# Optimization experiments

Measured on AMD Instinct MI355X. Metric: run time of the kernel, lower is better.

## Reference

```python
import jax, jax.numpy as jnp
import numpy as np

N = 50000; E = 800000; IN = 256; HID = 128; H = 4; C = 32; L = 3
REL = 100; RD = 16; EH = 32  # rel_emb_dim, edge-encoder hidden
LN_EPS = 1e-5


def _ln(x, g, b):
    m = jnp.mean(x, axis=-1, keepdims=True)
    v = jnp.mean((x - m) ** 2, axis=-1, keepdims=True)
    return (x - m) * jax.lax.rsqrt(v + LN_EPS) * g + b


def _mlp2(x, W1, b1, W2, b2):
    return jax.nn.relu(x @ W1 + b1) @ W2 + b2


def _forward(x, edge_attr, in_g, in_b, proj_W, proj_b,
             dist_W1, dist_b1, dist_W2, dist_b2,
             coexp_W1, coexp_b1, coexp_W2, coexp_b2,
             rel_emb, fus_W1, fus_b1, fus_ln_g, fus_ln_b, fus_W2, fus_b2,
             Wsrc, Wdst, Wedge, att, sscale, ng, nb, edge_index):
    src, dst = edge_index[0], edge_index[1]
    dist_w = edge_attr[:, 0]                              # [E] raw distance weight
    # ---- edge encoder ----
    dist_feat = _mlp2(edge_attr[:, 0:1], dist_W1, dist_b1, dist_W2, dist_b2)   # [E,RD]
    coexp_feat = _mlp2(edge_attr[:, 1:2], coexp_W1, coexp_b1, coexp_W2, coexp_b2)
    rel_id = jnp.clip(edge_attr[:, 2].astype(jnp.int32), 0, REL - 1)
    rel_feat = rel_emb[rel_id]                            # [E,RD]
    comb = jnp.concatenate([dist_feat, coexp_feat, rel_feat], axis=1)          # [E,3*RD]
    h = comb @ fus_W1 + fus_b1
    h = jax.nn.relu(_ln(h, fus_ln_g, fus_ln_b))
    edge_feat = h @ fus_W2 + fus_b2                       # [E,RD]
    # ---- input norm + projection ----
    x = _ln(x, in_g, in_b) @ proj_W + proj_b              # [N,HID]
    # ---- GAT layers ----
    for i in range(L):
        x_res = x
        xs = (x @ Wsrc[i]).reshape(N, H, C)
        xd = (x @ Wdst[i]).reshape(N, H, C)
        ef = (edge_feat @ Wedge[i]).reshape(E, H, C)
        a = jnp.tanh(xs[src] + xd[dst] + ef)              # [E,H,C]
        alpha = jnp.sum(a * att[i][None], axis=-1)        # [E,H]
        if i < L - 1:  # spatial_decay on all but last layer
            alpha = alpha * (dist_w[:, None] ** sscale[i][None, :])
        amax = jax.ops.segment_max(alpha, dst, num_segments=N)   # [N,H]
        ea = jnp.exp(alpha - amax[dst])
        esum = jax.ops.segment_sum(ea, dst, num_segments=N)
        alpha = ea / (esum[dst] + 1e-8)                   # [E,H]
        msg = xs[src] * alpha[..., None]                  # [E,H,C]
        out = jax.ops.segment_sum(msg, dst, num_segments=N).reshape(N, H * C)
        x = jax.nn.elu(_ln(out, ng[i], nb[i])) + x_res
    return x


def setup_inputs() -> dict:
    key = jax.random.key(0)
    ks = jax.random.split(key, 24)
    p = lambda k, s: jax.random.normal(k, s, jnp.float32) * 0.05
    edge_attr = jnp.concatenate([
        jax.random.uniform(ks[2], (E, 2), jnp.float32, 0.01, 1.0),
        jax.random.randint(ks[3], (E, 1), 0, REL).astype(jnp.float32)], axis=1)
    return dict(
        x=jax.random.normal(ks[0], (N, IN), jnp.float32),
        edge_index=jax.random.randint(ks[1], (2, E), 0, N),
        edge_attr=edge_attr,
        in_g=jnp.ones((IN,), jnp.float32), in_b=jnp.zeros((IN,), jnp.float32),
        proj_W=p(ks[4], (IN, HID)), proj_b=jnp.zeros((HID,), jnp.float32),
        dist_W1=p(ks[5], (1, EH)), dist_b1=jnp.zeros((EH,), jnp.float32),
        dist_W2=p(ks[6], (EH, RD)), dist_b2=jnp.zeros((RD,), jnp.float32),
        coexp_W1=p(ks[7], (1, EH)), coexp_b1=jnp.zeros((EH,), jnp.float32),
        coexp_W2=p(ks[8], (EH, RD)), coexp_b2=jnp.zeros((RD,), jnp.float32),
        rel_emb=p(ks[9], (REL, RD)),
        fus_W1=p(ks[10], (3 * RD, 2 * RD)), fus_b1=jnp.zeros((2 * RD,), jnp.float32),
        fus_ln_g=jnp.ones((2 * RD,), jnp.float32), fus_ln_b=jnp.zeros((2 * RD,), jnp.float32),
        fus_W2=p(ks[11], (2 * RD, RD)), fus_b2=jnp.zeros((RD,), jnp.float32),
        Wsrc=p(ks[12], (L, HID, HID)), Wdst=p(ks[13], (L, HID, HID)),
        Wedge=p(ks[14], (L, RD, HID)), att=p(ks[15], (L, H, C)),
        sscale=jnp.ones((L, H), jnp.float32),
        ng=jnp.ones((L, HID), jnp.float32), nb=jnp.zeros((L, HID), jnp.float32),
    )


def reference(x, edge_index, edge_attr, in_g, in_b, proj_W, proj_b,
              dist_W1, dist_b1, dist_W2, dist_b2,
              coexp_W1, coexp_b1, coexp_W2, coexp_b2,
              rel_emb, fus_W1, fus_b1, fus_ln_g, fus_ln_b, fus_W2, fus_b2,
              Wsrc, Wdst, Wedge, att, sscale, ng, nb):
    return _forward(x, edge_attr, in_g, in_b, proj_W, proj_b,
                    dist_W1, dist_b1, dist_W2, dist_b2,
                    coexp_W1, coexp_b1, coexp_W2, coexp_b2,
                    rel_emb, fus_W1, fus_b1, fus_ln_g, fus_ln_b, fus_W2, fus_b2,
                    Wsrc, Wdst, Wedge, att, sscale, ng, nb, edge_index)
```

## Files before the change

kernel.cpp:

```cpp
#include <hip/hip_runtime.h>
#include <math.h>

#define NN 50000
#define NE 800000
#define IND 256
#define HD 128
#define NH 4
#define NC 32
#define RELN 100
#define RD 16
#define EHD 32

typedef unsigned int uint;
typedef _Float16 half2_t __attribute__((ext_vector_type(2)));

__device__ inline uint pack_bf16(float a, float b) {
    uint ua = __float_as_uint(a), ub = __float_as_uint(b);
    ua += 0x7fffu + ((ua >> 16) & 1u);
    ub += 0x7fffu + ((ub >> 16) & 1u);
    return (ua >> 16) | (ub & 0xffff0000u);
}

__device__ inline uint pack_f16(float a, float b) {
    half2_t h = { (_Float16)a, (_Float16)b };
    return __builtin_bit_cast(uint, h);
}

#if __has_builtin(__builtin_amdgcn_fdot2)
#define FDOT2(a, b, c) __builtin_amdgcn_fdot2((a), (b), (c), false)
#else
static __device__ inline float FDOT2(half2_t a, half2_t b, float c) {
    return c + (float)a.x * (float)b.x + (float)a.y * (float)b.y;
}
#endif

__device__ inline float dpp_add(float a, const int ctrl) {
    int t;
    switch (ctrl) {
        case 0: t = __builtin_amdgcn_update_dpp(0, __float_as_int(a), 0xB1,  0xF, 0xF, true); break;
        case 1: t = __builtin_amdgcn_update_dpp(0, __float_as_int(a), 0x4E,  0xF, 0xF, true); break;
        case 2: t = __builtin_amdgcn_update_dpp(0, __float_as_int(a), 0x141, 0xF, 0xF, true); break;
        default:t = __builtin_amdgcn_update_dpp(0, __float_as_int(a), 0x140, 0xF, 0xF, true); break;
    }
    return a + __int_as_float(t);
}
__device__ inline float dpp_reduce16(float a) {
    a = dpp_add(a, 0);
    a = dpp_add(a, 1);
    a = dpp_add(a, 2);
    a = dpp_add(a, 3);
    return a;
}

__global__ __launch_bounds__(256) void count_kernel(
    const int* __restrict__ dst, int* __restrict__ counts)
{
    int e = blockIdx.x * 256 + threadIdx.x;
    if (e < NE) atomicAdd(&counts[dst[e]], 1);
}

__global__ __launch_bounds__(1024) void scan_a_kernel(
    const int* __restrict__ counts, int* __restrict__ row_ptr,
    int* __restrict__ partials, int n)
{
    __shared__ int wsum[16];
    int tid = threadIdx.x;
    int i = blockIdx.x * 1024 + tid;
    int v = (i < n) ? counts[i] : 0;
    int lane = tid & 63;
    int incl = v;
#pragma unroll
    for (int off = 1; off < 64; off <<= 1) {
        int t = __shfl_up(incl, off);
        if (lane >= off) incl += t;
    }
    if (lane == 63) wsum[tid >> 6] = incl;
    __syncthreads();
    if (tid < 16) {
        int w = wsum[tid];
        int inc2 = w;
#pragma unroll
        for (int off = 1; off < 16; off <<= 1) {
            int u = __shfl_up(inc2, off);
            if (tid >= off) inc2 += u;
        }
        wsum[tid] = inc2 - w;
    }
    __syncthreads();
    int excl = wsum[tid >> 6] + incl - v;
    if (i < n) row_ptr[i] = excl;
    if (tid == 1023) partials[blockIdx.x] = excl + v;
}

__global__ __launch_bounds__(64) void scan_b_kernel(
    int* __restrict__ partials, int* __restrict__ row_ptr, int nblk, int n)
{
    int tid = threadIdx.x;
    int v = (tid < nblk) ? partials[tid] : 0;
    int incl = v;
#pragma unroll
    for (int off = 1; off < 64; off <<= 1) {
        int t = __shfl_up(incl, off);
        if (tid >= off) incl += t;
    }
    if (tid < nblk) partials[tid] = incl - v;
    if (tid == nblk - 1) row_ptr[n] = incl;
}

__global__ __launch_bounds__(1024) void scan_c_kernel(
    int* __restrict__ row_ptr, int* __restrict__ cursor,
    const int* __restrict__ partials, int n)
{
    int i = blockIdx.x * 1024 + threadIdx.x;
    if (i < n) {
        int r = row_ptr[i] + partials[blockIdx.x];
        row_ptr[i] = r;
        cursor[i] = r;
    }
}

__global__ __launch_bounds__(256) void edge_feat_fill_kernel(
    const float* __restrict__ eattr, const int* __restrict__ src,
    const int* __restrict__ dst, int* __restrict__ cursor,
    const float* __restrict__ dW1, const float* __restrict__ db1,
    const float* __restrict__ dW2, const float* __restrict__ db2,
    const float* __restrict__ cW1, const float* __restrict__ cb1,
    const float* __restrict__ cW2, const float* __restrict__ cb2,
    const float* __restrict__ rel_emb,
    const float* __restrict__ fW1, const float* __restrict__ fb1,
    const float* __restrict__ fg,  const float* __restrict__ fbl,
    const float* __restrict__ fW2, const float* __restrict__ fb2,
    uint4* __restrict__ efeat_h, int2* __restrict__ meta_c)
{
    int e = blockIdx.x * 256 + threadIdx.x;
    if (e >= NE) return;
    float d  = eattr[(size_t)e * 3 + 0];
    float cx = eattr[(size_t)e * 3 + 1];
    int r = (int)eattr[(size_t)e * 3 + 2];
    r = min(max(r, 0), RELN - 1);
    int p = atomicAdd(&cursor[dst[e]], 1);
    meta_c[p] = make_int2(src[e], __float_as_int(__log2f(d)));

    float df[RD], cf[RD];
#pragma unroll
    for (int k = 0; k < RD; k++) { df[k] = db2[k]; cf[k] = cb2[k]; }
    for (int j = 0; j < EHD; j++) {
        float h1 = fmaxf(d  * dW1[j] + db1[j], 0.f);
        float h2 = fmaxf(cx * cW1[j] + cb1[j], 0.f);
#pragma unroll
        for (int k = 0; k < RD; k++) {
            df[k] += h1 * dW2[j * RD + k];
            cf[k] += h2 * cW2[j * RD + k];
        }
    }
    float hh[2 * RD];
#pragma unroll
    for (int m = 0; m < 2 * RD; m++) hh[m] = fb1[m];
    for (int k = 0; k < RD; k++) {
        float a = df[k], b = cf[k], c = rel_emb[r * RD + k];
#pragma unroll
        for (int m = 0; m < 2 * RD; m++) {
            hh[m] += a * fW1[k * (2 * RD) + m]
                   + b * fW1[(RD + k) * (2 * RD) + m]
                   + c * fW1[(2 * RD + k) * (2 * RD) + m];
        }
    }
    float s = 0.f;
#pragma unroll
    for (int m = 0; m < 2 * RD; m++) s += hh[m];
    float mean = s * (1.f / (2 * RD));
    float s2 = 0.f;
#pragma unroll
    for (int m = 0; m < 2 * RD; m++) { float dd = hh[m] - mean; s2 += dd * dd; }
    float rs = rsqrtf(s2 * (1.f / (2 * RD)) + 1e-5f);
#pragma unroll
    for (int m = 0; m < 2 * RD; m++)
        hh[m] = fmaxf((hh[m] - mean) * rs * fg[m] + fbl[m], 0.f);

    float ef[RD];
#pragma unroll
    for (int k = 0; k < RD; k++) ef[k] = fb2[k];
    for (int m = 0; m < 2 * RD; m++) {
        float hv = hh[m];
#pragma unroll
        for (int k = 0; k < RD; k++) ef[k] += hv * fW2[m * RD + k];
    }
    uint4 e0, e1;
    e0.x = pack_f16(ef[0],  ef[1]);  e0.y = pack_f16(ef[2],  ef[3]);
    e0.z = pack_f16(ef[4],  ef[5]);  e0.w = pack_f16(ef[6],  ef[7]);
    e1.x = pack_f16(ef[8],  ef[9]);  e1.y = pack_f16(ef[10], ef[11]);
    e1.z = pack_f16(ef[12], ef[13]); e1.w = pack_f16(ef[14], ef[15]);
    efeat_h[(size_t)p * 2 + 0] = e0;
    efeat_h[(size_t)p * 2 + 1] = e1;
}

__global__ __launch_bounds__(256) void ln_proj_kernel(
    const float* __restrict__ x, const float* __restrict__ g, const float* __restrict__ b,
    const float* __restrict__ W, const float* __restrict__ pb, float* __restrict__ x0)
{
    __shared__ float xr[8][IND];
    __shared__ float mv[8][2];
    int nb = blockIdx.x * 8;
    int tid = threadIdx.x;
    const float4* xv = (const float4*)(x + (size_t)nb * IND);
    float4* xl = (float4*)&xr[0][0];
    xl[tid] = xv[tid];
    xl[tid + 256] = xv[tid + 256];
    __syncthreads();
    int node = tid >> 5, lane = tid & 31;
    float s1 = 0.f, s2 = 0.f;
#pragma unroll
    for (int j = 0; j < 8; j++) { float v = xr[node][lane + 32 * j]; s1 += v; s2 += v * v; }
#pragma unroll
    for (int off = 16; off >= 1; off >>= 1) { s1 += __shfl_xor(s1, off); s2 += __shfl_xor(s2, off); }
    if (lane == 0) {
        float mean = s1 * (1.f / IND);
        mv[node][0] = mean;
        mv[node][1] = rsqrtf(s2 * (1.f / IND) - mean * mean + 1e-5f);
    }
    __syncthreads();
#pragma unroll
    for (int j = 0; j < 8; j++) {
        int k = lane + 32 * j;
        xr[node][k] = (xr[node][k] - mv[node][0]) * mv[node][1] * g[k] + b[k];
    }
    __syncthreads();
    int col = tid & 127, r0 = (tid >> 7) * 4;
    float acc[4] = {0.f, 0.f, 0.f, 0.f};
    for (int k = 0; k < IND; k += 4) {
        float4 x4[4];
#pragma unroll
        for (int r = 0; r < 4; r++) x4[r] = *(const float4*)&xr[r0 + r][k];
        float w0 = W[(k + 0) * HD + col];
        float w1 = W[(k + 1) * HD + col];
        float w2 = W[(k + 2) * HD + col];
        float w3 = W[(k + 3) * HD + col];
#pragma unroll
        for (int r = 0; r < 4; r++)
            acc[r] += x4[r].x * w0 + x4[r].y * w1 + x4[r].z * w2 + x4[r].w * w3;
    }
    float pbv = pb[col];
#pragma unroll
    for (int r = 0; r < 4; r++)
        x0[(size_t)(nb + r0 + r) * HD + col] = acc[r] + pbv;
}

__global__ __launch_bounds__(512) void gemm_sd_kernel(
    const float* __restrict__ x, const float* __restrict__ Ws, const float* __restrict__ Wd,
    uint* __restrict__ xs_p, float2* __restrict__ xd2)
{
    __shared__ float xt[32][HD];
    int nb = blockIdx.x * 32;
    int tid = threadIdx.x;
    const float4* xv = (const float4*)(x + (size_t)nb * HD);
    float4* xl = (float4*)&xt[0][0];
    int validf4 = (NN - nb >= 32) ? 1024 : (NN - nb) * 32;
#pragma unroll
    for (int u = 0; u < 2; u++) {
        int idx = tid + u * 512;
        float4 v = {0.f, 0.f, 0.f, 0.f};
        if (idx < validf4) v = xv[idx];
        xl[idx] = v;
    }
    __syncthreads();
    int half = tid >> 8;
    int t = tid & 255;
    int q = t & 31;
    int r0 = (t >> 5) * 4;
    const float4* W4 = (const float4*)(half ? Wd : Ws);
    float4 acc[4] = { {0,0,0,0}, {0,0,0,0}, {0,0,0,0}, {0,0,0,0} };
    for (int k = 0; k < HD; k += 4) {
        float4 xr[4];
#pragma unroll
        for (int r = 0; r < 4; r++) xr[r] = *(const float4*)&xt[r0 + r][k];
        float4 w0 = W4[(k + 0) * 32 + q];
        float4 w1 = W4[(k + 1) * 32 + q];
        float4 w2 = W4[(k + 2) * 32 + q];
        float4 w3 = W4[(k + 3) * 32 + q];
#pragma unroll
        for (int r = 0; r < 4; r++) {
            acc[r].x += xr[r].x * w0.x + xr[r].y * w1.x + xr[r].z * w2.x + xr[r].w * w3.x;
            acc[r].y += xr[r].x * w0.y + xr[r].y * w1.y + xr[r].z * w2.y + xr[r].w * w3.y;
            acc[r].z += xr[r].x * w0.z + xr[r].y * w1.z + xr[r].z * w2.z + xr[r].w * w3.z;
            acc[r].w += xr[r].x * w0.w + xr[r].y * w1.w + xr[r].z * w2.w + xr[r].w * w3.w;
        }
    }
    if (half == 0) {
#pragma unroll
        for (int r = 0; r < 4; r++) {
            int n = nb + r0 + r;
            if (n < NN) {
                uint2 pk;
                pk.x = pack_bf16(acc[r].x, acc[r].y);
                pk.y = pack_bf16(acc[r].z, acc[r].w);
                *(uint2*)&xs_p[(size_t)n * 64 + 2 * q] = pk;
            }
        }
    } else {
#pragma unroll
        for (int r = 0; r < 4; r++) {
            int n = nb + r0 + r;
            if (n < NN) {
                float2* o = &xd2[(size_t)n * 64 + 2 * q];
                o[0] = make_float2(acc[r].x, acc[r].y);
                o[1] = make_float2(acc[r].z, acc[r].w);
            }
        }
    }
}

__global__ __launch_bounds__(256) void aggregate_kernel(
    const uint* __restrict__ xs_p, const float2* __restrict__ xd2,
    const uint4* __restrict__ efeat_h, const int2* __restrict__ meta_c,
    const int* __restrict__ row_ptr,
    const float* __restrict__ Wedge_i, const float2* __restrict__ att2,
    const float* __restrict__ sscale_i, const float2* __restrict__ ng2,
    const float2* __restrict__ nb2, float2* __restrict__ xio2,
    int apply_dist, int nwaves)
{
    int l = threadIdx.x & 63;
    int wid = blockIdx.x * 4 + __builtin_amdgcn_readfirstlane(threadIdx.x >> 6);

    int c0 = 2 * l, c1 = 2 * l + 1;
    half2_t wxh[8], wyh[8];
#pragma unroll
    for (int q = 0; q < 8; q++) {
        wxh[q] = (half2_t){ (_Float16)Wedge_i[(2 * q) * HD + c0],
                            (_Float16)Wedge_i[(2 * q + 1) * HD + c0] };
        wyh[q] = (half2_t){ (_Float16)Wedge_i[(2 * q) * HD + c1],
                            (_Float16)Wedge_i[(2 * q + 1) * HD + c1] };
    }
    float2 attv = att2[l];
    float sc = sscale_i[l >> 4];
    float2 g = ng2[l], bb = nb2[l];

    auto loadB = [&](int b, int e1, int2* mt, uint* xw, uint4 (*ef)[2]) {
#pragma unroll
        for (int j = 0; j < 4; j++) {
            int pp = min(b + j, e1 - 1);
            mt[j] = meta_c[pp];
            ef[j][0] = efeat_h[(size_t)pp * 2 + 0];
            ef[j][1] = efeat_h[(size_t)pp * 2 + 1];
        }
#pragma unroll
        for (int j = 0; j < 4; j++) xw[j] = xs_p[(size_t)mt[j].x * 64 + l];
    };

    auto computeB = [&](int b, int e1, const int2* mt, const uint* xw,
                        const uint4 (*ef)[2], float2 xdv,
                        float& esum, float2& macc) {
#pragma unroll
        for (int j = 0; j < 4; j++) {
            const half2_t* eh = (const half2_t*)&ef[j][0];
            float efx = 0.f, efy = 0.f;
#pragma unroll
            for (int q = 0; q < 8; q++) {
                efx = FDOT2(eh[q], wxh[q], efx);
                efy = FDOT2(eh[q], wyh[q], efy);
            }
            float xvx = __uint_as_float(xw[j] << 16);
            float xvy = __uint_as_float(xw[j] & 0xffff0000u);
            float zx = xvx + xdv.x + efx;
            float zy = xvy + xdv.y + efy;
            float tx = 1.f - 2.f * __builtin_amdgcn_rcpf(__expf(2.f * zx) + 1.f);
            float ty = 1.f - 2.f * __builtin_amdgcn_rcpf(__expf(2.f * zy) + 1.f);
            float a = tx * attv.x + ty * attv.y;
            a = dpp_reduce16(a);
            if (apply_dist) a *= exp2f(__int_as_float(mt[j].y) * sc);
            float ea = __expf(a);
            ea = (b + j < e1) ? ea : 0.f;
            esum += ea;
            macc.x += xvx * ea;
            macc.y += xvy * ea;
        }
    };

    auto epilogue = [&](int node, float esum, float2 macc, float2 xres) {
        float inv = __builtin_amdgcn_rcpf(esum + 1e-8f);
        float2 outv = { macc.x * inv, macc.y * inv };
        float s1 = outv.x + outv.y;
        float s2 = outv.x * outv.x + outv.y * outv.y;
#pragma unroll
        for (int off = 32; off >= 1; off >>= 1) { s1 += __shfl_xor(s1, off); s2 += __shfl_xor(s2, off); }
        float mean = s1 * (1.f / HD);
        float var = s2 * (1.f / HD) - mean * mean;
        float rstd = rsqrtf(var + 1e-5f);
        float yx = (outv.x - mean) * rstd * g.x + bb.x;
        float yy = (outv.y - mean) * rstd * g.y + bb.y;
        float ex = (yx > 0.f) ? yx : expm1f(yx);
        float ey = (yy > 0.f) ? yy : expm1f(yy);
        float2 res;
        res.x = ex + xres.x;
        res.y = ey + xres.y;
        xio2[(size_t)node * 64 + l] = res;
    };

    int node = wid;
    if (node >= NN) return;
    int e0 = row_ptr[node], e1 = row_ptr[node + 1];
    float2 xdv  = xd2[(size_t)node * 64 + l];
    float2 xres = xio2[(size_t)node * 64 + l];
    int2 mt[4], mtn[4];
    uint xw[4], xwn[4];
    uint4 ef[4][2], efn[4][2];
    if (e0 < e1) loadB(e0, e1, mt, xw, ef);
    float esum = 0.f;
    float2 macc = {0.f, 0.f};

    while (true) {
        int b = e0;
#pragma unroll 2
        for (; b + 4 < e1; b += 4) {
            loadB(b + 4, e1, mtn, xwn, efn);
            __builtin_amdgcn_sched_barrier(0);
            computeB(b, e1, mt, xw, ef, xdv, esum, macc);
#pragma unroll
            for (int j = 0; j < 4; j++) {
                mt[j] = mtn[j]; xw[j] = xwn[j];
                ef[j][0] = efn[j][0]; ef[j][1] = efn[j][1];
            }
        }
        int nnode = node + nwaves;
        int ne0 = 0, ne1 = 0;
        float2 nxdv = {0.f, 0.f}, nxres = {0.f, 0.f};
        if (nnode < NN) {
            ne0 = row_ptr[nnode]; ne1 = row_ptr[nnode + 1];
            nxdv  = xd2[(size_t)nnode * 64 + l];
            nxres = xio2[(size_t)nnode * 64 + l];
            if (ne0 < ne1) loadB(ne0, ne1, mtn, xwn, efn);
        }
        __builtin_amdgcn_sched_barrier(0);
        if (b < e1) computeB(b, e1, mt, xw, ef, xdv, esum, macc);
        epilogue(node, esum, macc, xres);
        if (nnode >= NN) break;
        node = nnode; e0 = ne0; e1 = ne1; xdv = nxdv; xres = nxres;
        esum = 0.f; macc = make_float2(0.f, 0.f);
#pragma unroll
        for (int j = 0; j < 4; j++) {
            mt[j] = mtn[j]; xw[j] = xwn[j];
            ef[j][0] = efn[j][0]; ef[j][1] = efn[j][1];
        }
    }
}

extern "C" void kernel_launch(void* const* d_in, const int* in_sizes, int n_in,
                              void* d_out, int out_size, void* d_ws, size_t ws_size,
                              hipStream_t stream)
{
    const float* x_in   = (const float*)d_in[0];
    const int*   eidx   = (const int*)  d_in[1];
    const float* eattr  = (const float*)d_in[2];
    const float* in_g   = (const float*)d_in[3];
    const float* in_b   = (const float*)d_in[4];
    const float* proj_W = (const float*)d_in[5];
    const float* proj_b = (const float*)d_in[6];
    const float* dW1    = (const float*)d_in[7];
    const float* db1    = (const float*)d_in[8];
    const float* dW2    = (const float*)d_in[9];
    const float* db2    = (const float*)d_in[10];
    const float* cW1    = (const float*)d_in[11];
    const float* cb1    = (const float*)d_in[12];
    const float* cW2    = (const float*)d_in[13];
    const float* cb2    = (const float*)d_in[14];
    const float* rel_emb= (const float*)d_in[15];
    const float* fW1    = (const float*)d_in[16];
    const float* fb1    = (const float*)d_in[17];
    const float* fg     = (const float*)d_in[18];
    const float* fbl    = (const float*)d_in[19];
    const float* fW2    = (const float*)d_in[20];
    const float* fb2    = (const float*)d_in[21];
    const float* Wsrc   = (const float*)d_in[22];
    const float* Wdst   = (const float*)d_in[23];
    const float* Wedge  = (const float*)d_in[24];
    const float* att    = (const float*)d_in[25];
    const float* sscale = (const float*)d_in[26];
    const float* ng     = (const float*)d_in[27];
    const float* nb     = (const float*)d_in[28];

    const int* src = eidx;
    const int* dst = eidx + NE;

    char* p = (char*)d_ws;
    auto alloc = [&](size_t bytes) -> void* {
        void* r = p;
        p += (bytes + 255) & ~(size_t)255;
        return r;
    };
    uint*  xs_p    = (uint*) alloc((size_t)NN * 64 * 4);
    float* xd      = (float*)alloc((size_t)NN * HD * 4);
    uint4* efeat_h = (uint4*)alloc((size_t)NE * 32);
    int*   counts  = (int*)  alloc((size_t)NN * 4);
    int*   row_ptr = (int*)  alloc(((size_t)NN + 1) * 4);
    int*   cursor  = (int*)  alloc((size_t)NN * 4);
    int2*  meta_c  = (int2*) alloc((size_t)NE * 8);
    int*   partials= (int*)  alloc(256);

    float* x_cur = (float*)d_out;

    const int SCAN_NBLK = (NN + 1023) / 1024;

    hipMemsetAsync(counts, 0, (size_t)NN * 4, stream);
    hipLaunchKernelGGL(count_kernel, dim3(NE / 256), dim3(256), 0, stream, dst, counts);
    hipLaunchKernelGGL(scan_a_kernel, dim3(SCAN_NBLK), dim3(1024), 0, stream,
        counts, row_ptr, partials, NN);
    hipLaunchKernelGGL(scan_b_kernel, dim3(1), dim3(64), 0, stream,
        partials, row_ptr, SCAN_NBLK, NN);
    hipLaunchKernelGGL(scan_c_kernel, dim3(SCAN_NBLK), dim3(1024), 0, stream,
        row_ptr, cursor, partials, NN);
    hipLaunchKernelGGL(edge_feat_fill_kernel, dim3(NE / 256), dim3(256), 0, stream,
        eattr, src, dst, cursor, dW1, db1, dW2, db2, cW1, cb1, cW2, cb2, rel_emb,
        fW1, fb1, fg, fbl, fW2, fb2, efeat_h, meta_c);
    hipLaunchKernelGGL(ln_proj_kernel, dim3(NN / 8), dim3(256), 0, stream,
        x_in, in_g, in_b, proj_W, proj_b, x_cur);

    const int AGG_BLOCKS = 2048;
    const int NWAVES = AGG_BLOCKS * 4;
    for (int i = 0; i < 3; i++) {
        hipLaunchKernelGGL(gemm_sd_kernel, dim3((NN + 31) / 32), dim3(512), 0, stream,
            x_cur, Wsrc + (size_t)i * HD * HD, Wdst + (size_t)i * HD * HD,
            xs_p, (float2*)xd);
        hipLaunchKernelGGL(aggregate_kernel, dim3(AGG_BLOCKS), dim3(256), 0, stream,
            xs_p, (const float2*)xd, efeat_h, meta_c, row_ptr,
            Wedge + (size_t)i * RD * HD, (const float2*)(att + (size_t)i * NH * NC),
            sscale + (size_t)i * NH,
            (const float2*)(ng + (size_t)i * HD), (const float2*)(nb + (size_t)i * HD),
            (float2*)x_cur, (i < 2) ? 1 : 0, NWAVES);
    }
}
```

Before: 781.1 us.

## Partition GAT layer work by edge count with contiguous node ranges per wave

Each wave now binary-searches row_ptr to own a contiguous range of destination nodes holding roughly an equal share of edges, replacing the old node-strided assignment, to balance load across waves with skewed degrees. Padding entries are appended to meta_c and efeat_h so that batch loads may read past a row end without clamping, which removes the min() per load. The tanh and softmax exponentials are rewritten as exp2 with prescaled constants and an fma. The cost is two binary searches per wave and reliance on zeroed padding for reads beyond the last edge.

```diff
diff --git a/kernel.cpp b/kernel.cpp
--- a/kernel.cpp
+++ b/kernel.cpp
@@ -133,6 +133,12 @@
     uint4* __restrict__ efeat_h, int2* __restrict__ meta_c)
 {
     int e = blockIdx.x * 256 + threadIdx.x;
+    if (e < 8) {
+        meta_c[NE + e] = make_int2(0, 0);
+        uint4 z = {0u, 0u, 0u, 0u};
+        efeat_h[(size_t)(NE + e) * 2 + 0] = z;
+        efeat_h[(size_t)(NE + e) * 2 + 1] = z;
+    }
     if (e >= NE) return;
     float d  = eattr[(size_t)e * 3 + 0];
     float cx = eattr[(size_t)e * 3 + 1];
@@ -334,13 +340,22 @@
     float sc = sscale_i[l >> 4];
     float2 g = ng2[l], bb = nb2[l];
 
-    auto loadB = [&](int b, int e1, int2* mt, uint* xw, uint4 (*ef)[2]) {
+    int t0 = (int)((long long)wid * NE / nwaves);
+    int t1 = (int)((long long)(wid + 1) * NE / nwaves);
+    int lo = 0, hi = NN;
+    while (lo < hi) { int mid = (lo + hi) >> 1; if (row_ptr[mid] < t0) lo = mid + 1; else hi = mid; }
+    int nlo = lo;
+    hi = NN;
+    while (lo < hi) { int mid = (lo + hi) >> 1; if (row_ptr[mid] < t1) lo = mid + 1; else hi = mid; }
+    int nhi = (wid == nwaves - 1) ? NN : lo;
+    if (nlo >= nhi) return;
+
+    auto loadB = [&](int b, int2* mt, uint* xw, uint4 (*ef)[2]) {
 #pragma unroll
         for (int j = 0; j < 4; j++) {
-            int pp = min(b + j, e1 - 1);
-            mt[j] = meta_c[pp];
-            ef[j][0] = efeat_h[(size_t)pp * 2 + 0];
-            ef[j][1] = efeat_h[(size_t)pp * 2 + 1];
+            mt[j] = meta_c[b + j];
+            ef[j][0] = efeat_h[(size_t)(b + j) * 2 + 0];
+            ef[j][1] = efeat_h[(size_t)(b + j) * 2 + 1];
         }
 #pragma unroll
         for (int j = 0; j < 4; j++) xw[j] = xs_p[(size_t)mt[j].x * 64 + l];
@@ -362,12 +377,14 @@
             float xvy = __uint_as_float(xw[j] & 0xffff0000u);
             float zx = xvx + xdv.x + efx;
             float zy = xvy + xdv.y + efy;
-            float tx = 1.f - 2.f * __builtin_amdgcn_rcpf(__expf(2.f * zx) + 1.f);
-            float ty = 1.f - 2.f * __builtin_amdgcn_rcpf(__expf(2.f * zy) + 1.f);
+            float px = exp2f(zx * 2.88539008f);
+            float py = exp2f(zy * 2.88539008f);
+            float tx = __builtin_fmaf(-2.f, __builtin_amdgcn_rcpf(px + 1.f), 1.f);
+            float ty = __builtin_fmaf(-2.f, __builtin_amdgcn_rcpf(py + 1.f), 1.f);
             float a = tx * attv.x + ty * attv.y;
             a = dpp_reduce16(a);
             if (apply_dist) a *= exp2f(__int_as_float(mt[j].y) * sc);
-            float ea = __expf(a);
+            float ea = exp2f(a * 1.44269504f);
             ea = (b + j < e1) ? ea : 0.f;
             esum += ea;
             macc.x += xvx * ea;
@@ -395,15 +412,14 @@
         xio2[(size_t)node * 64 + l] = res;
     };
 
-    int node = wid;
-    if (node >= NN) return;
+    int node = nlo;
     int e0 = row_ptr[node], e1 = row_ptr[node + 1];
     float2 xdv  = xd2[(size_t)node * 64 + l];
     float2 xres = xio2[(size_t)node * 64 + l];
     int2 mt[4], mtn[4];
     uint xw[4], xwn[4];
     uint4 ef[4][2], efn[4][2];
-    if (e0 < e1) loadB(e0, e1, mt, xw, ef);
+    if (e0 < e1) loadB(e0, mt, xw, ef);
     float esum = 0.f;
     float2 macc = {0.f, 0.f};
 
@@ -411,7 +427,7 @@
         int b = e0;
 #pragma unroll 2
         for (; b + 4 < e1; b += 4) {
-            loadB(b + 4, e1, mtn, xwn, efn);
+            loadB(b + 4, mtn, xwn, efn);
             __builtin_amdgcn_sched_barrier(0);
             computeB(b, e1, mt, xw, ef, xdv, esum, macc);
 #pragma unroll
@@ -420,19 +436,19 @@
                 ef[j][0] = efn[j][0]; ef[j][1] = efn[j][1];
             }
         }
-        int nnode = node + nwaves;
+        int nnode = node + 1;
         int ne0 = 0, ne1 = 0;
         float2 nxdv = {0.f, 0.f}, nxres = {0.f, 0.f};
-        if (nnode < NN) {
-            ne0 = row_ptr[nnode]; ne1 = row_ptr[nnode + 1];
+        if (nnode < nhi) {
+            ne0 = e1; ne1 = row_ptr[nnode + 1];
             nxdv  = xd2[(size_t)nnode * 64 + l];
             nxres = xio2[(size_t)nnode * 64 + l];
-            if (ne0 < ne1) loadB(ne0, ne1, mtn, xwn, efn);
+            if (ne0 < ne1) loadB(ne0, mtn, xwn, efn);
         }
         __builtin_amdgcn_sched_barrier(0);
         if (b < e1) computeB(b, e1, mt, xw, ef, xdv, esum, macc);
         epilogue(node, esum, macc, xres);
-        if (nnode >= NN) break;
+        if (nnode >= nhi) break;
         node = nnode; e0 = ne0; e1 = ne1; xdv = nxdv; xres = nxres;
         esum = 0.f; macc = make_float2(0.f, 0.f);
 #pragma unroll
@@ -488,11 +504,11 @@
     };
     uint*  xs_p    = (uint*) alloc((size_t)NN * 64 * 4);
     float* xd      = (float*)alloc((size_t)NN * HD * 4);
-    uint4* efeat_h = (uint4*)alloc((size_t)NE * 32);
+    uint4* efeat_h = (uint4*)alloc((size_t)(NE + 8) * 32);
     int*   counts  = (int*)  alloc((size_t)NN * 4);
     int*   row_ptr = (int*)  alloc(((size_t)NN + 1) * 4);
     int*   cursor  = (int*)  alloc((size_t)NN * 4);
-    int2*  meta_c  = (int2*) alloc((size_t)NE * 8);
+    int2*  meta_c  = (int2*) alloc((size_t)(NE + 8) * 8);
     int*   partials= (int*)  alloc(256);
 
     float* x_cur = (float*)d_out;
```

Result: slower. 822.4 us (+5.3%).
